# Kernel optimization log

Hardware: AMD Instinct MI355X
Metric: run time of the kernel (lower is better)

The kernel has to match this reference:

```python
import jax, jax.numpy as jnp
import numpy as np

B, IN, H = 4096, 1024, 1024

def setup_inputs() -> dict:
    key = jax.random.key(0)
    ks = jax.random.split(key, 7)
    s_in = 1.0 / np.sqrt(IN)
    s_h = 1.0 / np.sqrt(H)
    return {
        "x": jax.random.normal(ks[0], (B, IN), dtype=jnp.float32),
        "h": jax.random.normal(ks[1], (B, H), dtype=jnp.float32),
        "W_ih": jax.random.uniform(ks[2], (3 * H, IN), jnp.float32, -s_in, s_in),
        "b_ih": jax.random.uniform(ks[3], (3 * H,), jnp.float32, -s_in, s_in),
        "W_rzh": jax.random.uniform(ks[4], (2 * H, H), jnp.float32, -s_h, s_h),
        "W_nh": jax.random.uniform(ks[5], (H, H), jnp.float32, -s_h, s_h),
        "b_nh": jax.random.uniform(ks[6], (H,), jnp.float32, -s_h, s_h),
    }


def reference(x, h, W_ih, b_ih, W_rzh, W_nh, b_nh):
    # Input projection: one fused matmul producing (B, 3H)
    x_proj = x @ W_ih.T + b_ih
    r_x, z_x, n_x = jnp.split(x_proj, 3, axis=-1)
    # Fused r/z hidden projection (B, 2H)
    rz_h = h @ W_rzh.T
    r_h, z_h = jnp.split(rz_h, 2, axis=-1)
    r = jax.nn.sigmoid(r_x + r_h)
    z = jax.nn.sigmoid(z_x + z_h)
    n = jnp.tanh(n_x + r * (h @ W_nh.T + b_nh))
    return (1.0 - z) * n + z * h
```

## Files before the change

kernel.cpp:

```cpp
#include <hip/hip_runtime.h>
#include <hip/hip_bf16.h>
#include <stdint.h>


typedef __attribute__((ext_vector_type(8))) short bfrag8;
typedef __attribute__((ext_vector_type(16))) float f32x16;

__device__ __forceinline__ unsigned short f2bf(float f) {
  union { float f; unsigned u; } v; v.f = f;
  unsigned u = v.u;
  return (unsigned short)((u + 0x7fffu + ((u >> 16) & 1u)) >> 16);
}

__device__ __forceinline__ void load_lds16(const void* g, void* l) {
  __builtin_amdgcn_global_load_lds(
      (const __attribute__((address_space(1))) void*)g,
      (__attribute__((address_space(3))) void*)l, 16, 0, 0);
}

__device__ __forceinline__ void cvt8(const float* __restrict__ src,
                                     unsigned short* __restrict__ dst) {
  float4 f0 = ((const float4*)src)[0];
  float4 f1 = ((const float4*)src)[1];
  uint4 o;
  o.x = (unsigned)f2bf(f0.x) | ((unsigned)f2bf(f0.y) << 16);
  o.y = (unsigned)f2bf(f0.z) | ((unsigned)f2bf(f0.w) << 16);
  o.z = (unsigned)f2bf(f1.x) | ((unsigned)f2bf(f1.y) << 16);
  o.w = (unsigned)f2bf(f1.z) | ((unsigned)f2bf(f1.w) << 16);
  *(uint4*)dst = o;
}

__global__ void prep_all(const float* __restrict__ x, const float* __restrict__ h,
                         const float* __restrict__ W_ih, const float* __restrict__ W_rzh,
                         const float* __restrict__ W_nh,
                         unsigned short* __restrict__ A2, unsigned short* __restrict__ Wb) {
  int idx = blockIdx.x * blockDim.x + threadIdx.x;
  if (idx < (1 << 20)) {
    int j = idx << 3;
    int b = j >> 11;
    int c = j & 2047;
    const float* src = (c < 1024) ? (x + (size_t)b * 1024 + c)
                                  : (h + (size_t)b * 1024 + (c - 1024));
    cvt8(src, A2 + j);
  } else {
    int j2 = (idx - (1 << 20)) << 3;
    int row = j2 >> 11;
    int c = j2 & 2047;
    int g = row >> 5;
    int s = g & 3;
    int jc = ((g >> 2) << 5) + (row & 31);
    const float* src = nullptr;
    if (s == 0)      src = (c < 1024) ? (W_ih + (size_t)jc * 1024 + c)
                                      : (W_rzh + (size_t)jc * 1024 + (c - 1024));
    else if (s == 1) src = (c < 1024) ? (W_ih + (size_t)(1024 + jc) * 1024 + c)
                                      : (W_rzh + (size_t)(1024 + jc) * 1024 + (c - 1024));
    else if (s == 2) { if (c < 1024)  src = W_ih + (size_t)(2048 + jc) * 1024 + c; }
    else             { if (c >= 1024) src = W_nh + (size_t)jc * 1024 + (c - 1024); }
    if (src) cvt8(src, Wb + j2);
  }
}

__global__ __launch_bounds__(256, 2)
void gru_gemm_fused(const unsigned short* __restrict__ A2,
                    const unsigned short* __restrict__ Wb,
                    const float* __restrict__ h,
                    const float* __restrict__ b_ih,
                    const float* __restrict__ b_nh,
                    float* __restrict__ out) {
  __shared__ unsigned short ldsA[2 * 256 * 32];
  __shared__ unsigned short ldsB[6 * 32 * 32];

  const int lane = threadIdx.x & 63;
  const int wave = threadIdx.x >> 6;
  const int row0 = blockIdx.x << 8;
  const int bn = blockIdx.y;

  const int wm = wave << 6;
  const int m32 = lane & 31;
  const int khalf = lane >> 5;

  const int lrow = lane >> 2;
  const int lq = lane & 3;
  const int sq = lq ^ ((lrow >> 1) & 3);

  const unsigned short* gA[2][4];
  unsigned short* lA[2][4];
#pragma unroll
  for (int win = 0; win < 2; ++win)
#pragma unroll
    for (int ci = 0; ci < 4; ++ci) {
      gA[win][ci] = A2 + (size_t)(row0 + wm + ci * 16 + lrow) * 2048 + win * 1024 + sq * 8;
      lA[win][ci] = &ldsA[win * 8192 + (wm + ci * 16) * 32];
    }

  const int item_win[6] = {0, 0, 0, 1, 1, 1};
  const int item_s[6]   = {0, 1, 2, 0, 1, 3};
  const unsigned short* gB[3];
  unsigned short* lB[3];
#pragma unroll
  for (int i = 0; i < 3; ++i) {
    int j = wave * 3 + i;
    int item = j >> 1;
    int half = j & 1;
    gB[i] = Wb + (size_t)(bn * 128 + item_s[item] * 32 + half * 16 + lrow) * 2048
              + item_win[item] * 1024 + sq * 8;
    lB[i] = &ldsB[item * 1024 + half * 16 * 32];
  }

  f32x16 acc[2][4] = {};

  for (int k0 = 0; k0 < 1024; k0 += 32) {
    __syncthreads();
#pragma unroll
    for (int win = 0; win < 2; ++win)
#pragma unroll
      for (int ci = 0; ci < 4; ++ci) load_lds16(gA[win][ci] + k0, lA[win][ci]);
#pragma unroll
    for (int i = 0; i < 3; ++i) load_lds16(gB[i] + k0, lB[i]);
    __syncthreads();

#pragma unroll
    for (int ks = 0; ks < 2; ++ks) {
      const int pc = ((ks * 2 + khalf) ^ ((m32 >> 1) & 3)) * 8;
      bfrag8 a0[2], a1[2], bfr[6];
#pragma unroll
      for (int t = 0; t < 2; ++t) {
        a0[t] = *(const bfrag8*)&ldsA[(wm + t * 32 + m32) * 32 + pc];
        a1[t] = *(const bfrag8*)&ldsA[8192 + (wm + t * 32 + m32) * 32 + pc];
      }
#pragma unroll
      for (int it = 0; it < 6; ++it)
        bfr[it] = *(const bfrag8*)&ldsB[it * 1024 + m32 * 32 + pc];

#pragma unroll
      for (int t = 0; t < 2; ++t) {
        acc[t][0] = __builtin_amdgcn_mfma_f32_32x32x16_bf16(a0[t], bfr[0], acc[t][0], 0, 0, 0);
        acc[t][0] = __builtin_amdgcn_mfma_f32_32x32x16_bf16(a1[t], bfr[3], acc[t][0], 0, 0, 0);
        acc[t][1] = __builtin_amdgcn_mfma_f32_32x32x16_bf16(a0[t], bfr[1], acc[t][1], 0, 0, 0);
        acc[t][1] = __builtin_amdgcn_mfma_f32_32x32x16_bf16(a1[t], bfr[4], acc[t][1], 0, 0, 0);
        acc[t][2] = __builtin_amdgcn_mfma_f32_32x32x16_bf16(a0[t], bfr[2], acc[t][2], 0, 0, 0);
        acc[t][3] = __builtin_amdgcn_mfma_f32_32x32x16_bf16(a1[t], bfr[5], acc[t][3], 0, 0, 0);
      }
    }
  }

  const int jcol = bn * 32 + m32;
  const float br  = b_ih[jcol];
  const float bz  = b_ih[1024 + jcol];
  const float bnv = b_ih[2048 + jcol];
  const float bh  = b_nh[jcol];

#pragma unroll
  for (int t = 0; t < 2; ++t) {
#pragma unroll
    for (int i = 0; i < 16; ++i) {
      int mrow = row0 + wm + t * 32 + (i & 3) + ((i >> 2) << 3) + (khalf << 2);
      size_t off = (size_t)mrow * 1024 + jcol;
      float rg = 1.f / (1.f + __expf(-(acc[t][0][i] + br)));
      float zg = 1.f / (1.f + __expf(-(acc[t][1][i] + bz)));
      float e2 = __expf(2.f * (acc[t][2][i] + bnv + rg * (acc[t][3][i] + bh)));
      float ng = 1.f - 2.f / (e2 + 1.f);
      float hv = h[off];
      out[off] = ng + zg * (hv - ng);
    }
  }
}

extern "C" void kernel_launch(void* const* d_in, const int* in_sizes, int n_in,
                              void* d_out, int out_size, void* d_ws, size_t ws_size,
                              hipStream_t stream) {
  const float* x     = (const float*)d_in[0];
  const float* h     = (const float*)d_in[1];
  const float* W_ih  = (const float*)d_in[2];
  const float* b_ih  = (const float*)d_in[3];
  const float* W_rzh = (const float*)d_in[4];
  const float* W_nh  = (const float*)d_in[5];
  const float* b_nh  = (const float*)d_in[6];
  float* out = (float*)d_out;

  unsigned short* A2 = (unsigned short*)d_ws;
  unsigned short* Wb = A2 + (size_t)4096 * 2048;

  prep_all<<<dim3(8192), dim3(256), 0, stream>>>(x, h, W_ih, W_rzh, W_nh, A2, Wb);
  gru_gemm_fused<<<dim3(16, 32), dim3(256), 0, stream>>>(A2, Wb, h, b_ih, b_nh, out);
}
```

Baseline: 168.2 us.

## Pre-pack operands into MFMA fragment order and drop zero-padded weight blocks

```diff
diff --git a/kernel.cpp b/kernel.cpp
--- a/kernel.cpp
+++ b/kernel.cpp
@@ -33,42 +33,48 @@
 __global__ void prep_all(const float* __restrict__ x, const float* __restrict__ h,
                          const float* __restrict__ W_ih, const float* __restrict__ W_rzh,
                          const float* __restrict__ W_nh,
-                         unsigned short* __restrict__ A2, unsigned short* __restrict__ Wb) {
+                         unsigned short* __restrict__ A2t, unsigned short* __restrict__ Wbt) {
   int idx = blockIdx.x * blockDim.x + threadIdx.x;
   if (idx < (1 << 20)) {
-    int j = idx << 3;
-    int b = j >> 11;
-    int c = j & 2047;
-    const float* src = (c < 1024) ? (x + (size_t)b * 1024 + c)
-                                  : (h + (size_t)b * 1024 + (c - 1024));
-    cvt8(src, A2 + j);
+    int L = idx & 63;
+    int kc = (idx >> 6) & 63;
+    int win = (idx >> 12) & 1;
+    int T = idx >> 13;
+    int row = T * 32 + (L & 31);
+    int col = kc * 16 + (L >> 5) * 8;
+    const float* src = (win ? h : x) + (size_t)row * 1024 + col;
+    cvt8(src, A2t + (size_t)idx * 8);
   } else {
-    int j2 = (idx - (1 << 20)) << 3;
-    int row = j2 >> 11;
-    int c = j2 & 2047;
-    int g = row >> 5;
-    int s = g & 3;
-    int jc = ((g >> 2) << 5) + (row & 31);
-    const float* src = nullptr;
-    if (s == 0)      src = (c < 1024) ? (W_ih + (size_t)jc * 1024 + c)
-                                      : (W_rzh + (size_t)jc * 1024 + (c - 1024));
-    else if (s == 1) src = (c < 1024) ? (W_ih + (size_t)(1024 + jc) * 1024 + c)
-                                      : (W_rzh + (size_t)(1024 + jc) * 1024 + (c - 1024));
-    else if (s == 2) { if (c < 1024)  src = W_ih + (size_t)(2048 + jc) * 1024 + c; }
-    else             { if (c >= 1024) src = W_nh + (size_t)jc * 1024 + (c - 1024); }
-    if (src) cvt8(src, Wb + j2);
+    int c2 = idx - (1 << 20);
+    int L = c2 & 63;
+    int kc = (c2 >> 6) & 63;
+    int rest = c2 >> 12;
+    int bn = rest / 6;
+    int item = rest - bn * 6;
+    int jc = bn * 32 + (L & 31);
+    int col = kc * 16 + (L >> 5) * 8;
+    const float* src;
+    switch (item) {
+      case 0:  src = W_ih  + (size_t)jc * 1024 + col; break;
+      case 1:  src = W_ih  + (size_t)(1024 + jc) * 1024 + col; break;
+      case 2:  src = W_ih  + (size_t)(2048 + jc) * 1024 + col; break;
+      case 3:  src = W_rzh + (size_t)jc * 1024 + col; break;
+      case 4:  src = W_rzh + (size_t)(1024 + jc) * 1024 + col; break;
+      default: src = W_nh  + (size_t)jc * 1024 + col; break;
+    }
+    cvt8(src, Wbt + (size_t)c2 * 8);
   }
 }
 
 __global__ __launch_bounds__(256, 2)
-void gru_gemm_fused(const unsigned short* __restrict__ A2,
-                    const unsigned short* __restrict__ Wb,
+void gru_gemm_fused(const unsigned short* __restrict__ A2t,
+                    const unsigned short* __restrict__ Wbt,
                     const float* __restrict__ h,
                     const float* __restrict__ b_ih,
                     const float* __restrict__ b_nh,
                     float* __restrict__ out) {
-  __shared__ unsigned short ldsA[2 * 256 * 32];
-  __shared__ unsigned short ldsB[6 * 32 * 32];
+  __shared__ unsigned short ldsA[8 * 2 * 2 * 512];
+  __shared__ unsigned short ldsB[6 * 2 * 512];
 
   const int lane = threadIdx.x & 63;
   const int wave = threadIdx.x >> 6;
@@ -79,58 +85,58 @@
   const int m32 = lane & 31;
   const int khalf = lane >> 5;
 
-  const int lrow = lane >> 2;
-  const int lq = lane & 3;
-  const int sq = lq ^ ((lrow >> 1) & 3);
+  const unsigned short* gA[2][2][2];
+  unsigned short* lA[2][2][2];
+#pragma unroll
+  for (int t = 0; t < 2; ++t)
+#pragma unroll
+    for (int win = 0; win < 2; ++win)
+#pragma unroll
+      for (int kcl = 0; kcl < 2; ++kcl) {
+        int T = blockIdx.x * 8 + wave * 2 + t;
+        gA[t][win][kcl] = A2t + (size_t)(T * 2 + win) * 32768 + kcl * 512 + lane * 8;
+        lA[t][win][kcl] = &ldsA[(((wave * 2 + t) * 2 + win) * 2 + kcl) * 512];
+      }
 
-  const unsigned short* gA[2][4];
-  unsigned short* lA[2][4];
-#pragma unroll
-  for (int win = 0; win < 2; ++win)
-#pragma unroll
-    for (int ci = 0; ci < 4; ++ci) {
-      gA[win][ci] = A2 + (size_t)(row0 + wm + ci * 16 + lrow) * 2048 + win * 1024 + sq * 8;
-      lA[win][ci] = &ldsA[win * 8192 + (wm + ci * 16) * 32];
-    }
-
-  const int item_win[6] = {0, 0, 0, 1, 1, 1};
-  const int item_s[6]   = {0, 1, 2, 0, 1, 3};
   const unsigned short* gB[3];
   unsigned short* lB[3];
 #pragma unroll
   for (int i = 0; i < 3; ++i) {
     int j = wave * 3 + i;
     int item = j >> 1;
-    int half = j & 1;
-    gB[i] = Wb + (size_t)(bn * 128 + item_s[item] * 32 + half * 16 + lrow) * 2048
-              + item_win[item] * 1024 + sq * 8;
-    lB[i] = &ldsB[item * 1024 + half * 16 * 32];
+    int kcl = j & 1;
+    gB[i] = Wbt + (size_t)(bn * 6 + item) * 32768 + kcl * 512 + lane * 8;
+    lB[i] = &ldsB[(item * 2 + kcl) * 512];
   }
 
   f32x16 acc[2][4] = {};
 
   for (int k0 = 0; k0 < 1024; k0 += 32) {
+    const size_t koff = (size_t)k0 * 32;
     __syncthreads();
 #pragma unroll
-    for (int win = 0; win < 2; ++win)
+    for (int t = 0; t < 2; ++t)
 #pragma unroll
-      for (int ci = 0; ci < 4; ++ci) load_lds16(gA[win][ci] + k0, lA[win][ci]);
+      for (int win = 0; win < 2; ++win)
 #pragma unroll
-    for (int i = 0; i < 3; ++i) load_lds16(gB[i] + k0, lB[i]);
+        for (int kcl = 0; kcl < 2; ++kcl)
+          load_lds16(gA[t][win][kcl] + koff, lA[t][win][kcl]);
+#pragma unroll
+    for (int i = 0; i < 3; ++i) load_lds16(gB[i] + koff, lB[i]);
     __syncthreads();
 
 #pragma unroll
     for (int ks = 0; ks < 2; ++ks) {
-      const int pc = ((ks * 2 + khalf) ^ ((m32 >> 1) & 3)) * 8;
+      const int fo = ks * 512 + lane * 8;
       bfrag8 a0[2], a1[2], bfr[6];
 #pragma unroll
       for (int t = 0; t < 2; ++t) {
-        a0[t] = *(const bfrag8*)&ldsA[(wm + t * 32 + m32) * 32 + pc];
-        a1[t] = *(const bfrag8*)&ldsA[8192 + (wm + t * 32 + m32) * 32 + pc];
+        a0[t] = *(const bfrag8*)&ldsA[((wave * 2 + t) * 2 + 0) * 1024 + fo];
+        a1[t] = *(const bfrag8*)&ldsA[((wave * 2 + t) * 2 + 1) * 1024 + fo];
       }
 #pragma unroll
       for (int it = 0; it < 6; ++it)
-        bfr[it] = *(const bfrag8*)&ldsB[it * 1024 + m32 * 32 + pc];
+        bfr[it] = *(const bfrag8*)&ldsB[it * 1024 + fo];
 
 #pragma unroll
       for (int t = 0; t < 2; ++t) {
@@ -178,9 +184,9 @@
   const float* b_nh  = (const float*)d_in[6];
   float* out = (float*)d_out;
 
-  unsigned short* A2 = (unsigned short*)d_ws;
-  unsigned short* Wb = A2 + (size_t)4096 * 2048;
+  unsigned short* A2t = (unsigned short*)d_ws;
+  unsigned short* Wbt = A2t + (size_t)(1 << 20) * 8;
 
-  prep_all<<<dim3(8192), dim3(256), 0, stream>>>(x, h, W_ih, W_rzh, W_nh, A2, Wb);
-  gru_gemm_fused<<<dim3(16, 32), dim3(256), 0, stream>>>(A2, Wb, h, b_ih, b_nh, out);
+  prep_all<<<dim3(7168), dim3(256), 0, stream>>>(x, h, W_ih, W_rzh, W_nh, A2t, Wbt);
+  gru_gemm_fused<<<dim3(16, 32), dim3(256), 0, stream>>>(A2t, Wbt, h, b_ih, b_nh, out);
 }
```

New measurement: 164.3 us. -2.3%, faster.
